# Kernel tuning notes

Hardware: AMD Instinct MI355X
Metric: run time of the kernel (lower is better)

The kernel has to match this reference:

```python
import jax, jax.numpy as jnp
import numpy as np
from jax import lax

B, H, W, C = 8, 64, 64, 256
OUT = 1024          # channels (final conv filters)
KS = 3              # kernel_size
GROUP_DIV = 1
N_GROUPS = C // GROUP_DIV  # 256 -> depthwise-style grouped convs
DN = ('NHWC', 'HWIO', 'NHWC')
EPS = 1e-5


def setup_inputs() -> dict:
    key = jax.random.key(0)
    ks = jax.random.split(key, 6)
    x = jax.random.normal(ks[0], (B, H, W, C), jnp.float32)
    w_spatial = jax.random.normal(ks[1], (B, KS, KS, C // N_GROUPS, C), jnp.float32) * 0.05
    w_pointwise = jax.random.normal(ks[2], (B, 1, 1, C // N_GROUPS, C), jnp.float32) * 0.05
    bias = jax.random.normal(ks[3], (B, C), jnp.float32) * 0.05
    conv_w = jax.random.normal(ks[4], (KS, KS, C, OUT), jnp.float32) * (1.0 / np.sqrt(KS * KS * C))
    conv_b = jnp.zeros((OUT,), jnp.float32)
    return {"x": x, "w_spatial": w_spatial, "w_pointwise": w_pointwise,
            "bias": bias, "conv_w": conv_w, "conv_b": conv_b}


def _instance_norm(x):
    # TF: (x - mean) / (std + eps), population std over H,W per sample/channel
    mean = jnp.mean(x, axis=(1, 2), keepdims=True)
    std = jnp.sqrt(jnp.mean((x - mean) ** 2, axis=(1, 2), keepdims=True))
    return (x - mean) / (std + EPS)


def _per_sample(xi, ws, wp, b):
    # xi: [H,W,C]; ws: [ks,ks,1,C]; wp: [1,1,1,C]; b: [C]
    y = lax.conv_general_dilated(xi[None], ws, (1, 1), 'SAME',
                                 dimension_numbers=DN,
                                 feature_group_count=N_GROUPS)
    y = lax.conv_general_dilated(y, wp, (1, 1), 'VALID',
                                 dimension_numbers=DN,
                                 feature_group_count=N_GROUPS) + b
    return y[0]


def reference(x, w_spatial, w_pointwise, bias, conv_w, conv_b):
    x = _instance_norm(x)
    # batched per-sample dynamic grouped spatial + pointwise conv
    x = jax.vmap(_per_sample)(x, w_spatial, w_pointwise, bias)  # [B,H,W,C]
    # shared 3x3 SAME conv C -> OUT with bias
    y = lax.conv_general_dilated(x, conv_w, (1, 1), 'SAME',
                                 dimension_numbers=DN) + conv_b
    return y
```

## Files before the change

kernel.cpp:

```cpp
#include <hip/hip_runtime.h>
#include <hip/hip_bf16.h>
#include <cstdint>
#include <cstddef>

constexpr int Bn   = 8;
constexpr int Hn   = 64;
constexpr int Wn   = 64;
constexpr int Cn   = 256;
constexpr int OUTC = 1024;
constexpr int HPAD = 66;
constexpr int WPAD = 66;
#define EPS 1e-5f

typedef __attribute__((ext_vector_type(16))) float f32x16;
typedef __bf16 bf16x8 __attribute__((ext_vector_type(8)));

__device__ __forceinline__ void gload_lds16(const void* g, void* l) {
    __builtin_amdgcn_global_load_lds(
        (__attribute__((address_space(1))) void*)g,
        (__attribute__((address_space(3))) void*)l,
        16, 0, 0);
}

__global__ __launch_bounds__(256) void k0_transpose_w(const float* __restrict__ conv_w,
                                                      __hip_bfloat16* __restrict__ wT) {
    __shared__ float tile[64][65];
    const int tap = blockIdx.x;
    const int ct  = blockIdx.y;
    const int ot  = blockIdx.z;
    const int t   = threadIdx.x;
    const int lo  = t & 63;
    const int cq  = t >> 6;

#pragma unroll
    for (int k = 0; k < 16; ++k) {
        int ci = k * 4 + cq;
        tile[lo][ci] = conv_w[((size_t)(tap * Cn + ct * 64 + ci)) * OUTC + ot * 64 + lo];
    }
    __syncthreads();
#pragma unroll
    for (int k = 0; k < 16; ++k) {
        int oo = k * 4 + cq;
        wT[((size_t)(tap * OUTC + ot * 64 + oo)) * Cn + ct * 64 + lo] =
            __float2bfloat16(tile[oo][lo]);
    }
}

__global__ __launch_bounds__(1024) void k1_stats_partial(const float* __restrict__ x,
                                                         float* __restrict__ ps,
                                                         float* __restrict__ pq) {
    __shared__ float sb[2][4][256];
    const int bh = blockIdx.x;
    const int tid = threadIdx.x;
    const int c = tid & 255;
    const int s = tid >> 8;
    const float* row = x + (size_t)bh * Wn * Cn + (size_t)s * 16 * Cn + c;
    float sm = 0.f, q = 0.f;
#pragma unroll
    for (int w = 0; w < 16; ++w) {
        float v = row[(size_t)w * Cn];
        sm += v; q += v * v;
    }
    sb[0][s][c] = sm; sb[1][s][c] = q;
    __syncthreads();
    if (s == 0) {
        float S = 0.f, Q = 0.f;
#pragma unroll
        for (int k = 0; k < 4; ++k) { S += sb[0][k][c]; Q += sb[1][k][c]; }
        ps[bh * Cn + c] = S;
        pq[bh * Cn + c] = Q;
    }
}

__global__ __launch_bounds__(1024) void k2_stats_final(const float* __restrict__ ps,
                                                       const float* __restrict__ pq,
                                                       float* __restrict__ scale,
                                                       float* __restrict__ shift) {
    __shared__ float sb[2][4][256];
    const int b = blockIdx.x;
    const int tid = threadIdx.x;
    const int c = tid & 255;
    const int qd = tid >> 8;
    float S = 0.f, Q = 0.f;
#pragma unroll 4
    for (int i = 0; i < 16; ++i) {
        int h = qd * 16 + i;
        S += ps[(b * Hn + h) * Cn + c];
        Q += pq[(b * Hn + h) * Cn + c];
    }
    sb[0][qd][c] = S; sb[1][qd][c] = Q;
    __syncthreads();
    if (qd == 0) {
        float s2 = 0.f, q2 = 0.f;
#pragma unroll
        for (int k = 0; k < 4; ++k) { s2 += sb[0][k][c]; q2 += sb[1][k][c]; }
        const float inv = 1.f / (float)(Hn * Wn);
        float mean = s2 * inv;
        float var  = fmaxf(q2 * inv - mean * mean, 0.f);
        float sc   = 1.f / (sqrtf(var) + EPS);
        scale[b * Cn + c] = sc;
        shift[b * Cn + c] = -mean * sc;
    }
}

__global__ __launch_bounds__(256) void k3_dwconv(const float* __restrict__ x,
                                                 const float* __restrict__ w_sp,
                                                 const float* __restrict__ w_pw,
                                                 const float* __restrict__ bias,
                                                 const float* __restrict__ scale,
                                                 const float* __restrict__ shift,
                                                 __hip_bfloat16* __restrict__ tpad) {
    const int bq = blockIdx.x;
    const int wq = bq & 3;
    const int bh = bq >> 2;
    const int b  = bh / HPAD;
    const int hp = bh - b * HPAD;
    const int c  = threadIdx.x;
    __hip_bfloat16* orow = tpad + ((size_t)(b * HPAD + hp)) * WPAD * Cn + c;
    const __hip_bfloat16 z = __float2bfloat16(0.f);

    if (hp == 0 || hp == HPAD - 1) {
        int wlo = wq * 17, whi = wlo + 17 < WPAD ? wlo + 17 : WPAD;
        for (int wp = wlo; wp < whi; ++wp) orow[(size_t)wp * Cn] = z;
        return;
    }
    const int h = hp - 1;
    const float sc = scale[b * Cn + c];
    const float sh = shift[b * Cn + c];
    float w9[9];
#pragma unroll
    for (int k = 0; k < 9; ++k) w9[k] = w_sp[(b * 9 + k) * Cn + c];
    const float pw = w_pw[b * Cn + c];
    const float bv = bias[b * Cn + c];
    const float* xb = x + (size_t)b * Hn * Wn * Cn + c;

    bool rv[3];
#pragma unroll
    for (int r = 0; r < 3; ++r) { int rr = h - 1 + r; rv[r] = (rr >= 0 && rr < Hn); }

    if (wq == 0) orow[0] = z;
    if (wq == 3) orow[(size_t)(WPAD - 1) * Cn] = z;

    const int w0 = wq * 16;
    float win[3][3];
#pragma unroll
    for (int r = 0; r < 3; ++r) {
        win[r][0] = (rv[r] && w0 > 0)
                    ? (xb[((size_t)(h - 1 + r) * Wn + (w0 - 1)) * Cn] * sc + sh) : 0.f;
        win[r][1] = rv[r] ? (xb[((size_t)(h - 1 + r) * Wn + w0) * Cn] * sc + sh) : 0.f;
    }
    for (int i = 0; i < 16; ++i) {
        const int w = w0 + i;
#pragma unroll
        for (int r = 0; r < 3; ++r)
            win[r][2] = (rv[r] && (w + 1) < Wn)
                        ? (xb[((size_t)(h - 1 + r) * Wn + (w + 1)) * Cn] * sc + sh) : 0.f;
        float y = 0.f;
#pragma unroll
        for (int r = 0; r < 3; ++r)
#pragma unroll
            for (int qq = 0; qq < 3; ++qq)
                y += win[r][qq] * w9[r * 3 + qq];
        orow[(size_t)(w + 1) * Cn] = __float2bfloat16(y * pw + bv);
#pragma unroll
        for (int r = 0; r < 3; ++r) { win[r][0] = win[r][1]; win[r][1] = win[r][2]; }
    }
}

constexpr int KSTEPS = 72;
constexpr int BUFSZ  = 32768;

__global__ __launch_bounds__(512, 2) void k4_gemm(const __hip_bfloat16* __restrict__ tpad,
                                                  const __hip_bfloat16* __restrict__ wT,
                                                  const float* __restrict__ conv_b,
                                                  float* __restrict__ out) {
    __shared__ __align__(16) char smem[4 * BUFSZ];

    const int tid  = threadIdx.x;
    const int lane = tid & 63;
    const int wv   = tid >> 6;
    const int wm   = wv >> 2;
    const int wn   = wv & 3;
    const int l31  = lane & 31;
    const int kh2  = lane >> 5;

    const int bid = blockIdx.x;
    const int mt  = (bid & 7) * 16 + ((bid >> 3) & 15);
    const int nt  = bid >> 7;
    const int pixbase = mt * 256;
    const int b       = mt >> 4;
    const int hbase   = (mt & 15) * 4;
    const int obase   = nt * 256;

    int aoff[2], boff[2];
#pragma unroll
    for (int j = 0; j < 2; ++j) {
        int u = j * 512 + tid;
        int r = u >> 3, p = u & 7;
        int l = p ^ (r & 7);
        int pix = 2 * r + (l >> 2);
        int hh  = hbase + (pix >> 6);
        int ww  = pix & 63;
        aoff[j] = ((b * HPAD + hh) * WPAD + ww) * Cn + (l & 3) * 8;
        boff[j] = (obase + 2 * r + (l >> 2)) * Cn + (l & 3) * 8;
    }

    auto stageS = [&](int s) {
        const int tap = s >> 3, ks = s & 7;
        const int kh  = tap / 3, kw = tap - 3 * kh;
        const __hip_bfloat16* aS = tpad + ((kh * WPAD + kw) * Cn + ks * 32);
        const __hip_bfloat16* bS = wT + (size_t)tap * (OUTC * Cn) + ks * 32;
        char* buf = smem + (s & 3) * BUFSZ;
        gload_lds16(aS + aoff[0], buf + (size_t)(0 * 512 + wv * 64) * 16);
        gload_lds16(aS + aoff[1], buf + (size_t)(1 * 512 + wv * 64) * 16);
        gload_lds16(bS + boff[0], buf + 16384 + (size_t)(0 * 512 + wv * 64) * 16);
        gload_lds16(bS + boff[1], buf + 16384 + (size_t)(1 * 512 + wv * 64) * 16);
    };

    f32x16 acc[4][2] = {};

    auto substep = [&](int t, bool dostage) {
        char* Ab = smem + (t & 3) * BUFSZ;
        char* Bb = Ab + 16384;
        bf16x8 bfr[2][2], af[4][2];
#pragma unroll
        for (int nf = 0; nf < 2; ++nf)
#pragma unroll
            for (int kk = 0; kk < 2; ++kk) {
                int o = wn * 64 + nf * 32 + l31;
                int r = o >> 1;
                int slot = (((o & 1) << 2) | (kk * 2 + kh2)) ^ (r & 7);
                bfr[nf][kk] = *(const bf16x8*)(Bb + r * 128 + slot * 16);
            }
#pragma unroll
        for (int mf = 0; mf < 4; ++mf)
#pragma unroll
            for (int kk = 0; kk < 2; ++kk) {
                int pix = wm * 128 + mf * 32 + l31;
                int r = pix >> 1;
                int slot = (((pix & 1) << 2) | (kk * 2 + kh2)) ^ (r & 7);
                af[mf][kk] = *(const bf16x8*)(Ab + r * 128 + slot * 16);
            }
        if (dostage) stageS(t + 2);
        __builtin_amdgcn_s_setprio(1);
#pragma unroll
        for (int mf = 0; mf < 4; ++mf)
#pragma unroll
            for (int nf = 0; nf < 2; ++nf)
#pragma unroll
                for (int kk = 0; kk < 2; ++kk)
                    acc[mf][nf] = __builtin_amdgcn_mfma_f32_32x32x16_bf16(
                        af[mf][kk], bfr[nf][kk], acc[mf][nf], 0, 0, 0);
        __builtin_amdgcn_s_setprio(0);
    };

    stageS(0);
    stageS(1);
    asm volatile("s_waitcnt vmcnt(0)" ::: "memory");
    __builtin_amdgcn_s_barrier();
    __builtin_amdgcn_sched_barrier(0);

#pragma unroll 1
    for (int body = 0; body < KSTEPS / 2; ++body) {
        const int t0 = 2 * body;
        substep(t0,     t0 + 2 < KSTEPS);
        substep(t0 + 1, t0 + 3 < KSTEPS);
        __builtin_amdgcn_sched_barrier(0);
        if (body + 1 < KSTEPS / 2) {
            asm volatile("s_waitcnt vmcnt(0)" ::: "memory");
            __builtin_amdgcn_s_barrier();
            __builtin_amdgcn_sched_barrier(0);
        }
    }

    float cb[2];
#pragma unroll
    for (int nf = 0; nf < 2; ++nf) cb[nf] = conv_b[obase + wn * 64 + nf * 32 + l31];
#pragma unroll
    for (int mf = 0; mf < 4; ++mf) {
#pragma unroll
        for (int j = 0; j < 16; ++j) {
            int row = (j & 3) + 8 * (j >> 2) + 4 * kh2;
            int r = pixbase + wm * 128 + mf * 32 + row;
            float* orow = out + (size_t)r * OUTC + obase + wn * 64 + l31;
            orow[0]  = acc[mf][0][j] + cb[0];
            orow[32] = acc[mf][1][j] + cb[1];
        }
    }
}

extern "C" void kernel_launch(void* const* d_in, const int* in_sizes, int n_in,
                              void* d_out, int out_size, void* d_ws, size_t ws_size,
                              hipStream_t stream) {
    const float* x      = (const float*)d_in[0];
    const float* w_sp   = (const float*)d_in[1];
    const float* w_pw   = (const float*)d_in[2];
    const float* bias   = (const float*)d_in[3];
    const float* conv_w = (const float*)d_in[4];
    const float* conv_b = (const float*)d_in[5];
    float* out = (float*)d_out;

    char* ws = (char*)d_ws;
    __hip_bfloat16* wT    = (__hip_bfloat16*)(ws);
    float*          ps    = (float*)(ws + 4718592);
    float*          pq    = (float*)(ws + 4718592 + 524288);
    float*          scale = (float*)(ws + 5767168);
    float*          shift = (float*)(ws + 5775360);
    __hip_bfloat16* tpad  = (__hip_bfloat16*)(ws + 5783552);

    k0_transpose_w<<<dim3(9, 4, 16), 256, 0, stream>>>(conv_w, wT);
    k1_stats_partial<<<Bn * Hn, 1024, 0, stream>>>(x, ps, pq);
    k2_stats_final<<<Bn, 1024, 0, stream>>>(ps, pq, scale, shift);
    k3_dwconv<<<Bn * HPAD * 4, 256, 0, stream>>>(x, w_sp, w_pw, bias, scale, shift, tpad);
    k4_gemm<<<512, 512, 0, stream>>>(tpad, wT, conv_b, out);
}
```

Before: 188.4 us.

## Stage GEMM tiles through registers instead of direct global-to-LDS loads

Replaces the global_load_lds direct-to-LDS staging in the main implicit-GEMM conv kernel with ordinary vector global loads into registers, followed by explicit LDS stores of a k-group-major layout with no swizzle. Loads for the next two stages are issued before the first substep and written to LDS between the two substeps, so the global latency is meant to overlap with MFMA work. This costs extra VGPRs and LDS store instructions. The unswizzled layout may also raise LDS bank conflicts on fragment reads.

```diff
diff --git a/kernel.cpp b/kernel.cpp
--- a/kernel.cpp
+++ b/kernel.cpp
@@ -12,15 +12,9 @@
 constexpr int WPAD = 66;
 #define EPS 1e-5f
 
+typedef __attribute__((ext_vector_type(4))) float f32x4;
 typedef __attribute__((ext_vector_type(16))) float f32x16;
 typedef __bf16 bf16x8 __attribute__((ext_vector_type(8)));
-
-__device__ __forceinline__ void gload_lds16(const void* g, void* l) {
-    __builtin_amdgcn_global_load_lds(
-        (__attribute__((address_space(1))) void*)g,
-        (__attribute__((address_space(3))) void*)l,
-        16, 0, 0);
-}
 
 __global__ __launch_bounds__(256) void k0_transpose_w(const float* __restrict__ conv_w,
                                                       __hip_bfloat16* __restrict__ wT) {
@@ -192,90 +186,103 @@
     const int hbase   = (mt & 15) * 4;
     const int obase   = nt * 256;
 
-    int aoff[2], boff[2];
-#pragma unroll
-    for (int j = 0; j < 2; ++j) {
-        int u = j * 512 + tid;
-        int r = u >> 3, p = u & 7;
-        int l = p ^ (r & 7);
-        int pix = 2 * r + (l >> 2);
-        int hh  = hbase + (pix >> 6);
-        int ww  = pix & 63;
-        aoff[j] = ((b * HPAD + hh) * WPAD + ww) * Cn + (l & 3) * 8;
-        boff[j] = (obase + 2 * r + (l >> 2)) * Cn + (l & 3) * 8;
-    }
-
-    auto stageS = [&](int s) {
+    const int srow  = tid >> 1;
+    const int shalf = tid & 1;
+    const int ahh = hbase + (srow >> 6);
+    const int aww = srow & 63;
+    const int aGbase = ((b * HPAD + ahh) * WPAD + aww) * Cn + shalf * 16;
+    const int bGbase = (obase + srow) * Cn + shalf * 16;
+    const int aDst = (2 * shalf) * 4096 + srow * 16;
+    const int bDst = 16384 + (2 * shalf) * 4096 + srow * 16;
+
+    auto issueLoads = [&](int s, bf16x8& a0, bf16x8& a1, bf16x8& b0, bf16x8& b1) {
         const int tap = s >> 3, ks = s & 7;
         const int kh  = tap / 3, kw = tap - 3 * kh;
-        const __hip_bfloat16* aS = tpad + ((kh * WPAD + kw) * Cn + ks * 32);
-        const __hip_bfloat16* bS = wT + (size_t)tap * (OUTC * Cn) + ks * 32;
+        const __hip_bfloat16* aS = tpad + (kh * WPAD + kw) * Cn + ks * 32 + aGbase;
+        const __hip_bfloat16* bS = wT + (size_t)tap * (OUTC * Cn) + ks * 32 + bGbase;
+        a0 = *(const bf16x8*)(aS);
+        a1 = *(const bf16x8*)(aS + 8);
+        b0 = *(const bf16x8*)(bS);
+        b1 = *(const bf16x8*)(bS + 8);
+    };
+    auto writeStage = [&](int s, bf16x8 a0, bf16x8 a1, bf16x8 b0, bf16x8 b1) {
         char* buf = smem + (s & 3) * BUFSZ;
-        gload_lds16(aS + aoff[0], buf + (size_t)(0 * 512 + wv * 64) * 16);
-        gload_lds16(aS + aoff[1], buf + (size_t)(1 * 512 + wv * 64) * 16);
-        gload_lds16(bS + boff[0], buf + 16384 + (size_t)(0 * 512 + wv * 64) * 16);
-        gload_lds16(bS + boff[1], buf + 16384 + (size_t)(1 * 512 + wv * 64) * 16);
+        *(bf16x8*)(buf + aDst)        = a0;
+        *(bf16x8*)(buf + aDst + 4096) = a1;
+        *(bf16x8*)(buf + bDst)        = b0;
+        *(bf16x8*)(buf + bDst + 4096) = b1;
     };
 
+    const int aRow = (wm * 128 + l31) * 16;
+    const int bRow = 16384 + (wn * 64 + l31) * 16;
+    const int kg0 = kh2 * 4096;
+    const int kg1 = (2 + kh2) * 4096;
+
     f32x16 acc[4][2] = {};
 
-    auto substep = [&](int t, bool dostage) {
-        char* Ab = smem + (t & 3) * BUFSZ;
-        char* Bb = Ab + 16384;
-        bf16x8 bfr[2][2], af[4][2];
-#pragma unroll
-        for (int nf = 0; nf < 2; ++nf)
-#pragma unroll
-            for (int kk = 0; kk < 2; ++kk) {
-                int o = wn * 64 + nf * 32 + l31;
-                int r = o >> 1;
-                int slot = (((o & 1) << 2) | (kk * 2 + kh2)) ^ (r & 7);
-                bfr[nf][kk] = *(const bf16x8*)(Bb + r * 128 + slot * 16);
-            }
-#pragma unroll
-        for (int mf = 0; mf < 4; ++mf)
-#pragma unroll
-            for (int kk = 0; kk < 2; ++kk) {
-                int pix = wm * 128 + mf * 32 + l31;
-                int r = pix >> 1;
-                int slot = (((pix & 1) << 2) | (kk * 2 + kh2)) ^ (r & 7);
-                af[mf][kk] = *(const bf16x8*)(Ab + r * 128 + slot * 16);
-            }
-        if (dostage) stageS(t + 2);
+    auto substep = [&](int t) {
+        char* buf = smem + (t & 3) * BUFSZ;
+        bf16x8 bfr[2][2], afr[4][2];
+#pragma unroll
+        for (int nf = 0; nf < 2; ++nf) {
+            bfr[nf][0] = *(const bf16x8*)(buf + bRow + nf * 512 + kg0);
+            bfr[nf][1] = *(const bf16x8*)(buf + bRow + nf * 512 + kg1);
+        }
+#pragma unroll
+        for (int mf = 0; mf < 4; ++mf) {
+            afr[mf][0] = *(const bf16x8*)(buf + aRow + mf * 512 + kg0);
+            afr[mf][1] = *(const bf16x8*)(buf + aRow + mf * 512 + kg1);
+        }
         __builtin_amdgcn_s_setprio(1);
 #pragma unroll
-        for (int mf = 0; mf < 4; ++mf)
-#pragma unroll
-            for (int nf = 0; nf < 2; ++nf)
-#pragma unroll
-                for (int kk = 0; kk < 2; ++kk)
+        for (int kk = 0; kk < 2; ++kk)
+#pragma unroll
+            for (int mf = 0; mf < 4; ++mf)
+#pragma unroll
+                for (int nf = 0; nf < 2; ++nf)
                     acc[mf][nf] = __builtin_amdgcn_mfma_f32_32x32x16_bf16(
-                        af[mf][kk], bfr[nf][kk], acc[mf][nf], 0, 0, 0);
+                        afr[mf][kk], bfr[nf][kk], acc[mf][nf], 0, 0, 0);
         __builtin_amdgcn_s_setprio(0);
     };
 
-    stageS(0);
-    stageS(1);
+    bf16x8 pa0, pa1, pb0, pb1, qa0, qa1, qb0, qb1;
+
+    issueLoads(0, pa0, pa1, pb0, pb1);
+    issueLoads(1, qa0, qa1, qb0, qb1);
     asm volatile("s_waitcnt vmcnt(0)" ::: "memory");
+    writeStage(0, pa0, pa1, pb0, pb1);
+    writeStage(1, qa0, qa1, qb0, qb1);
+    asm volatile("s_waitcnt lgkmcnt(0)" ::: "memory");
     __builtin_amdgcn_s_barrier();
     __builtin_amdgcn_sched_barrier(0);
 
 #pragma unroll 1
     for (int body = 0; body < KSTEPS / 2; ++body) {
         const int t0 = 2 * body;
-        substep(t0,     t0 + 2 < KSTEPS);
-        substep(t0 + 1, t0 + 3 < KSTEPS);
+        const bool st = (t0 + 2 < KSTEPS);
+        if (st) {
+            issueLoads(t0 + 2, pa0, pa1, pb0, pb1);
+            issueLoads(t0 + 3, qa0, qa1, qb0, qb1);
+        }
+        substep(t0);
+        __builtin_amdgcn_sched_barrier(0);
+        if (st) {
+            asm volatile("s_waitcnt vmcnt(0)" ::: "memory");
+            writeStage(t0 + 2, pa0, pa1, pb0, pb1);
+            writeStage(t0 + 3, qa0, qa1, qb0, qb1);
+        }
+        substep(t0 + 1);
         __builtin_amdgcn_sched_barrier(0);
         if (body + 1 < KSTEPS / 2) {
-            asm volatile("s_waitcnt vmcnt(0)" ::: "memory");
+            asm volatile("s_waitcnt lgkmcnt(0)" ::: "memory");
             __builtin_amdgcn_s_barrier();
             __builtin_amdgcn_sched_barrier(0);
         }
     }
 
-    float cb[2];
-#pragma unroll
-    for (int nf = 0; nf < 2; ++nf) cb[nf] = conv_b[obase + wn * 64 + nf * 32 + l31];
+    float cb2[2];
+#pragma unroll
+    for (int nf = 0; nf < 2; ++nf) cb2[nf] = conv_b[obase + wn * 64 + nf * 32 + l31];
 #pragma unroll
     for (int mf = 0; mf < 4; ++mf) {
 #pragma unroll
@@ -283,8 +290,8 @@
             int row = (j & 3) + 8 * (j >> 2) + 4 * kh2;
             int r = pixbase + wm * 128 + mf * 32 + row;
             float* orow = out + (size_t)r * OUTC + obase + wn * 64 + l31;
-            orow[0]  = acc[mf][0][j] + cb[0];
-            orow[32] = acc[mf][1][j] + cb[1];
+            orow[0]  = acc[mf][0][j] + cb2[0];
+            orow[32] = acc[mf][1][j] + cb2[1];
         }
     }
 }
```

Result: slower. 215.4 us (+14.3%).
